# Performance work log

Measured on AMD Instinct MI355X. Metric: run time of the kernel, lower is better.

Reference implementation:

```python
import jax, jax.numpy as jnp
import numpy as np

MAX_POS = 512  # hardcoded max_pos_emb in the module
LN_EPS = 1e-5


def setup_inputs() -> dict:
    key = jax.random.key(0)
    ks = jax.random.split(key, 6)
    bs, n, d = 16, 4000, 1024
    h, dh = 8, 128
    inner = h * dh
    return {
        "x": jax.random.normal(ks[0], (bs, n, d), jnp.float32),
        "ln_w": jnp.ones((d,), jnp.float32),
        "ln_b": jnp.zeros((d,), jnp.float32),
        "Wq": (jax.random.normal(ks[1], (inner, d), jnp.float32) * 0.02),
        "Wkv": (jax.random.normal(ks[2], (2 * inner, d), jnp.float32) * 0.02),
        "Wo": (jax.random.normal(ks[3], (d, inner), jnp.float32) * 0.02),
        "bo": jnp.zeros((d,), jnp.float32),
        "rel_emb": (jax.random.normal(ks[4], (2 * MAX_POS + 1, dh), jnp.float32) * 0.02),
        "context_size": 256,
    }


def reference(x, ln_w, ln_b, Wq, Wkv, Wo, bo, rel_emb, context_size):
    bs, n, d = x.shape
    dh = rel_emb.shape[1]
    h = Wq.shape[0] // dh
    scale = dh ** -0.5
    cs = int(context_size)
    nb = -(-n // cs)          # ceil(n / cs)
    nr = n % cs

    # pre_norm (LayerNorm)
    mu = jnp.mean(x, axis=-1, keepdims=True)
    var = jnp.var(x, axis=-1, keepdims=True)
    xn = (x - mu) * jax.lax.rsqrt(var + LN_EPS) * ln_w + ln_b
    if nr > 0:
        xn = jnp.pad(xn, ((0, 0), (0, cs - nr), (0, 0)))

    q = xn @ Wq.T                    # (bs, nb*cs, h*dh)
    k, v = jnp.split(xn @ Wkv.T, 2, axis=-1)

    def blk(t):  # -> (bs, nb, h, cs, dh)
        return t.reshape(bs, nb, cs, h, dh).transpose(0, 1, 3, 2, 4)

    q, k, v = blk(q), blk(k), blk(v)

    # relative position bias, computed as a GEMM instead of broadcast-mul-sum
    seq = jnp.arange(cs)
    dist = jnp.clip(seq[:, None] - seq[None, :], -cs, cs) + MAX_POS
    rel = rel_emb[dist]                                     # (cs, cs, dh)
    pos_attn = jnp.einsum('bnhid,ijd->bnhij', q, rel) * scale

    if nr > 0:
        m = np.ones((cs, cs), dtype=bool)
        m[:nr, :nr] = False
        neg = -jnp.finfo(pos_attn.dtype).max
        pos_attn = pos_attn.at[:, -1].set(
            jnp.where(jnp.asarray(m), neg, pos_attn[:, -1]))

    # SDPA with additive mask: softmax(q k^T * scale + pos_attn) v
    scores = jnp.einsum('bnhid,bnhjd->bnhij', q, k) * scale + pos_attn
    attn = jax.nn.softmax(scores, axis=-1)
    out = jnp.einsum('bnhij,bnhjd->bnhid', attn, v)         # (bs, nb, h, cs, dh)

    out = out.transpose(0, 1, 3, 2, 4).reshape(bs, nb * cs, h * dh)[:, :n]
    return out @ Wo.T + bo  # dropout is identity in eval
```

## Files before the change

kernel.cpp:

```cpp
#include <hip/hip_runtime.h>

typedef __bf16 bf16;
typedef __bf16 bf16x8 __attribute__((ext_vector_type(8)));
typedef float f32x4 __attribute__((ext_vector_type(4)));

#define MFMA16(A,B,C) __builtin_amdgcn_mfma_f32_16x16x32_bf16(A,B,C,0,0,0)
#define SCALE 0.08838834764831843f
#define NEGBIG (-1e30f)

#define AS1(p) ((__attribute__((address_space(1))) void*)(p))
#define AS3(p) ((__attribute__((address_space(3))) void*)(p))

#define BAR() do { asm volatile("" ::: "memory"); __builtin_amdgcn_s_barrier(); asm volatile("" ::: "memory"); } while (0)

__global__ void cvt_bf16(const float* __restrict__ src, bf16* __restrict__ dst, int n) {
    int i = (blockIdx.x * 256 + threadIdx.x) * 4;
    if (i < n) {
        float4 v = *(const float4*)(src + i);
        dst[i + 0] = (bf16)v.x; dst[i + 1] = (bf16)v.y;
        dst[i + 2] = (bf16)v.z; dst[i + 3] = (bf16)v.w;
    }
}

__global__ __launch_bounds__(256) void ln_kernel(const float* __restrict__ x,
                                                 const float* __restrict__ w,
                                                 const float* __restrict__ b,
                                                 bf16* __restrict__ xn) {
    int row = blockIdx.x;
    int bb = row >> 12, p = row & 4095;
    int t = threadIdx.x;
    bf16* out = xn + ((size_t)row << 10);
    if (p >= 4000) {
        uint2 z; z.x = 0u; z.y = 0u;
        *(uint2*)(out + t * 4) = z;
        return;
    }
    float4 v = *(const float4*)(x + (((size_t)bb * 4000 + p) << 10) + t * 4);
    float s = v.x + v.y + v.z + v.w;
    float s2 = v.x * v.x + v.y * v.y + v.z * v.z + v.w * v.w;
#pragma unroll
    for (int m = 1; m < 64; m <<= 1) { s += __shfl_xor(s, m); s2 += __shfl_xor(s2, m); }
    __shared__ float red[8];
    int wv = t >> 6, l = t & 63;
    if (l == 0) { red[wv] = s; red[4 + wv] = s2; }
    __syncthreads();
    s = red[0] + red[1] + red[2] + red[3];
    s2 = red[4] + red[5] + red[6] + red[7];
    float mu = s * (1.f / 1024.f);
    float var = s2 * (1.f / 1024.f) - mu * mu;
    float inv = rsqrtf(var + 1e-5f);
    float4 wv4 = *(const float4*)(w + t * 4);
    float4 bv4 = *(const float4*)(b + t * 4);
    union { bf16 h[4]; uint2 u; } o;
    o.h[0] = (bf16)((v.x - mu) * inv * wv4.x + bv4.x);
    o.h[1] = (bf16)((v.y - mu) * inv * wv4.y + bv4.y);
    o.h[2] = (bf16)((v.z - mu) * inv * wv4.z + bv4.z);
    o.h[3] = (bf16)((v.w - mu) * inv * wv4.w + bv4.w);
    *(uint2*)(out + t * 4) = o.u;
}


__device__ __forceinline__ void stage_half(const bf16* __restrict__ src, int srow, int K,
                                           int kofs, bf16* ldsb, int w, int l) {
#pragma unroll
    for (int r = 0; r < 2; ++r) {
        int rh = (r * 8 + w) * 8 + (l >> 3);
        int chunk = (l & 7) ^ (rh & 7);
        __builtin_amdgcn_global_load_lds(AS1(src + (size_t)(srow + rh) * K + kofs + chunk * 8),
                                         AS3(ldsb + (r * 8 + w) * 512), 16, 0, 0);
    }
}

__device__ __forceinline__ bf16x8 fragLD(const bf16* base, int row, int ks, int lk) {
    int ch = ((ks * 4 + lk) ^ (row & 7)) * 8;
    return *(const bf16x8*)(base + row * 64 + ch);
}

#define RDA(AF, base, mofs) \
    _Pragma("unroll") for (int m = 0; m < 4; ++m) \
    _Pragma("unroll") for (int ks = 0; ks < 2; ++ks) \
        AF[m][ks] = fragLD(base, rA + (mofs + m) * 16 + lrow, ks, lk);

#define RDB2(nb, base) \
    _Pragma("unroll") for (int n = 0; n < 2; ++n) \
    _Pragma("unroll") for (int ks = 0; ks < 2; ++ks) \
        bfr[(nb) + n][ks] = fragLD(base, rB + ((nb) + n) * 16 + lrow, ks, lk);

#define MM(mb, AF, nb) do { \
    __builtin_amdgcn_s_setprio(1); \
    _Pragma("unroll") for (int m = 0; m < 4; ++m) \
    _Pragma("unroll") for (int n = 0; n < 2; ++n) \
    _Pragma("unroll") for (int ks = 0; ks < 2; ++ks) \
        acc[(mb) + m][(nb) + n] = MFMA16(AF[m][ks], bfr[(nb) + n][ks], acc[(mb) + m][(nb) + n]); \
    __builtin_amdgcn_s_setprio(0); } while (0)

template <int EPI>
__global__ __launch_bounds__(512, 2) void gemm256(const bf16* __restrict__ A,
                                                  const bf16* __restrict__ B,
                                                  bf16* __restrict__ C,
                                                  float* __restrict__ Cf,
                                                  const float* __restrict__ bias,
                                                  int M, int N, int K) {
    __shared__ __align__(16) bf16 LA[2 * 16384];
    __shared__ __align__(16) bf16 LB[2 * 16384];
    const int t = threadIdx.x;
    const int w = t >> 6, l = t & 63;
    const int lrow = l & 15, lk = l >> 4;
    const int wrM = w >> 2, wn = w & 3;
    const int rA = wrM * 128, rB = wn * 64;

    const int nwg = gridDim.x, cpx = nwg >> 3;
    const int swz = ((int)blockIdx.x & 7) * cpx + ((int)blockIdx.x >> 3);
    const int nbk = N >> 8;
    const int m0 = (swz / nbk) * 256;
    const int n0 = (swz % nbk) * 256;

    bf16* LA0 = LA;          bf16* LB0 = LB;
    bf16* LA1 = LA + 16384;  bf16* LB1 = LB + 16384;

    f32x4 acc[8][4] = {};
    bf16x8 afL[4][2], afH[4][2], bfr[4][2];

    const int NT = K >> 6, NI = K >> 7;

    stage_half(B, n0,       K, 0,  LB0,        w, l);
    stage_half(B, n0 + 128, K, 0,  LB0 + 8192, w, l);
    stage_half(A, m0,       K, 0,  LA0,        w, l);
    stage_half(A, m0 + 128, K, 0,  LA0 + 8192, w, l);
    stage_half(B, n0,       K, 64, LB1,        w, l);
    stage_half(B, n0 + 128, K, 64, LB1 + 8192, w, l);
    stage_half(A, m0,       K, 64, LA1,        w, l);
    asm volatile("s_waitcnt vmcnt(6)" ::: "memory");
    BAR();

    for (int i = 0; i < NI; ++i) {
        const int kS1 = (2 * i + 1) << 6;
        const int t2 = 2 * i + 2, t3 = 2 * i + 3;
        const int kS2 = ((t2 < NT) ? t2 : NT - 1) << 6;
        const int kS3 = ((t3 < NT) ? t3 : NT - 1) << 6;

        RDA(afL, LA0, 0);
        if (wn < 2) { RDB2(0, LB0); RDB2(2, LB0); } else { RDB2(0, LB0); }
        stage_half(A, m0 + 128, K, kS1, LA1 + 8192, w, l);
        BAR();
        MM(0, afL, 0);
        BAR();
        if (wn >= 2) { RDB2(2, LB0); }
        stage_half(B, n0, K, kS2, LB0, w, l);
        BAR();
        MM(0, afL, 2);
        BAR();
        RDA(afH, LA0, 4);
        stage_half(B, n0 + 128, K, kS2, LB0 + 8192, w, l);
        BAR();
        MM(4, afH, 0);
        BAR();
        stage_half(A, m0, K, kS2, LA0, w, l);
        BAR();
        MM(4, afH, 2);
        asm volatile("s_waitcnt vmcnt(6)" ::: "memory");
        BAR();
        RDA(afL, LA1, 0);
        if (wn < 2) { RDB2(0, LB1); RDB2(2, LB1); } else { RDB2(0, LB1); }
        stage_half(A, m0 + 128, K, kS2, LA0 + 8192, w, l);
        BAR();
        MM(0, afL, 0);
        BAR();
        if (wn >= 2) { RDB2(2, LB1); }
        stage_half(B, n0, K, kS3, LB1, w, l);
        BAR();
        MM(0, afL, 2);
        BAR();
        RDA(afH, LA1, 4);
        stage_half(B, n0 + 128, K, kS3, LB1 + 8192, w, l);
        BAR();
        MM(4, afH, 0);
        BAR();
        stage_half(A, m0, K, kS3, LA1, w, l);
        BAR();
        MM(4, afH, 2);
        asm volatile("s_waitcnt vmcnt(6)" ::: "memory");
        BAR();
    }

    asm volatile("s_waitcnt vmcnt(0)" ::: "memory");

    if (EPI == 0) {
#pragma unroll
        for (int m = 0; m < 8; ++m)
#pragma unroll
            for (int r = 0; r < 4; ++r) {
                size_t row = (size_t)(m0 + rA + m * 16 + lk * 4 + r);
                bf16* dst = C + row * N + n0 + rB;
#pragma unroll
                for (int n = 0; n < 4; ++n) dst[n * 16 + lrow] = (bf16)acc[m][n][r];
            }
    } else {
#pragma unroll
        for (int m = 0; m < 8; ++m)
#pragma unroll
            for (int r = 0; r < 4; ++r) {
                int row = m0 + rA + m * 16 + lk * 4 + r;
                int p = row & 4095, bb2 = row >> 12;
                if (p < 4000) {
                    float* dst = Cf + ((size_t)bb2 * 4000 + p) * 1024 + n0 + rB;
#pragma unroll
                    for (int n = 0; n < 4; ++n)
                        dst[n * 16 + lrow] = acc[m][n][r] + bias[n0 + rB + n * 16 + lrow];
                }
            }
    }
}

__global__ __launch_bounds__(256, 2) void bias_skew(const bf16* __restrict__ qkv,
                                                    const bf16* __restrict__ relw,
                                                    bf16* __restrict__ skew) {
    int bidx = blockIdx.x;
    int g = bidx & 7, bb = bidx >> 3;
    int h = bb & 7, blkn = (bb >> 3) & 15, b = bb >> 7;
    int mrow0 = b * 4096 + blkn * 256 + g * 32;
    const int t = threadIdx.x, w = t >> 6, l = t & 63, lrow = l & 15, lk = l >> 4;
    __shared__ __align__(16) bf16 Qs[32 * 136];
    __shared__ __align__(16) bf16 Ws[32 * 520];

#pragma unroll
    for (int q = 0; q < 2; ++q) {
        int idx = q * 256 + t;
        int row = idx >> 4, c8 = idx & 15;
        bf16x8 v = *(const bf16x8*)(qkv + (size_t)(mrow0 + row) * 3072 + h * 128 + c8 * 8);
        *(bf16x8*)&Qs[row * 136 + c8 * 8] = v;
    }
    __syncthreads();

    f32x4 acc[2][8] = {};
#pragma unroll
    for (int ks = 0; ks < 4; ++ks) {
        bf16x8 aq0 = *(const bf16x8*)&Qs[lrow * 136 + ks * 32 + lk * 8];
        bf16x8 aq1 = *(const bf16x8*)&Qs[(16 + lrow) * 136 + ks * 32 + lk * 8];
#pragma unroll
        for (int ct = 0; ct < 8; ++ct) {
            int c = w * 128 + ct * 16 + lrow;
            bf16x8 br = *(const bf16x8*)(relw + (size_t)c * 128 + ks * 32 + lk * 8);
            acc[0][ct] = MFMA16(aq0, br, acc[0][ct]);
            acc[1][ct] = MFMA16(aq1, br, acc[1][ct]);
        }
    }
#pragma unroll
    for (int mt = 0; mt < 2; ++mt)
#pragma unroll
        for (int ct = 0; ct < 8; ++ct)
#pragma unroll
            for (int r = 0; r < 4; ++r)
                Ws[(mt * 16 + lk * 4 + r) * 520 + w * 128 + ct * 16 + lrow] =
                    (bf16)(acc[mt][ct][r] * SCALE);
    __syncthreads();

    int jt = t >> 6, ll = t & 63;
    bool last = (blkn == 15);
    const bf16 negbig = (bf16)NEGBIG;
    union { bf16 hh[32]; uint4 q4[4]; } ob;
#pragma unroll
    for (int e = 0; e < 32; ++e) {
        int mt = e >> 4, nt = (e >> 2) & 3, r = e & 3;
        int iloc = mt * 16 + (ll >> 4) * 4 + r;
        int j = jt * 64 + nt * 16 + (ll & 15);
        int ig = g * 32 + iloc;
        int c = ig - j + 255;
        bool masked = last && (ig >= 160 || j >= 160);
        ob.hh[e] = masked ? negbig : Ws[iloc * 520 + c];
    }
    uint4* dst = (uint4*)(skew + ((((size_t)bb * 8 + g) * 4 + jt) * 64 + ll) * 32);
#pragma unroll
    for (int qq = 0; qq < 4; ++qq) dst[qq] = ob.q4[qq];
}

__global__ __launch_bounds__(512, 2) void attn_kernel(const bf16* __restrict__ qkv,
                                                      const bf16* __restrict__ skew,
                                                      bf16* __restrict__ ao) {
    int bb = blockIdx.x;
    int h = bb & 7, blkn = (bb >> 3) & 15, b = bb >> 7;
    const int t = threadIdx.x, w = t >> 6, l = t & 63, lrow = l & 15, lk = l >> 4;
    size_t qrow0 = (size_t)(b * 4096 + blkn * 256);
    __shared__ __align__(16) bf16 Ks[64 * 136];
    __shared__ __align__(16) bf16 Vt[128 * 72];
    __shared__ __align__(16) bf16 Ps[8][32 * 72];

    int i0 = w * 32;
    bf16x8 aq[2][4];
#pragma unroll
    for (int mt = 0; mt < 2; ++mt)
#pragma unroll
        for (int ks = 0; ks < 4; ++ks)
            aq[mt][ks] = *(const bf16x8*)(qkv + (qrow0 + i0 + mt * 16 + lrow) * 3072 +
                                          h * 128 + ks * 32 + lk * 8);

    f32x4 o[2][8] = {};
    float mrun[2][4], lrun[2][4];
#pragma unroll
    for (int mt = 0; mt < 2; ++mt)
#pragma unroll
        for (int r = 0; r < 4; ++r) { mrun[mt][r] = NEGBIG; lrun[mt][r] = 0.f; }

    for (int jt = 0; jt < 4; ++jt) {
        __syncthreads();
#pragma unroll
        for (int q = 0; q < 2; ++q) {
            int idx = q * 512 + t;
            int row = idx >> 4, c8 = idx & 15;
            bf16x8 v = *(const bf16x8*)(qkv + (qrow0 + jt * 64 + row) * 3072 + 1024 +
                                        h * 128 + c8 * 8);
            *(bf16x8*)&Ks[row * 136 + c8 * 8] = v;
        }
#pragma unroll
        for (int q = 0; q < 2; ++q) {
            int idx = q * 512 + t;
            int row = idx >> 4, c8 = idx & 15;
            bf16x8 v = *(const bf16x8*)(qkv + (qrow0 + jt * 64 + row) * 3072 + 2048 +
                                        h * 128 + c8 * 8);
#pragma unroll
            for (int e = 0; e < 8; ++e) Vt[(c8 * 8 + e) * 72 + row] = v[e];
        }
        __syncthreads();

        f32x4 s[2][4] = {};
#pragma unroll
        for (int nt = 0; nt < 4; ++nt)
#pragma unroll
            for (int ks = 0; ks < 4; ++ks) {
                bf16x8 bk = *(const bf16x8*)&Ks[(nt * 16 + lrow) * 136 + ks * 32 + lk * 8];
                s[0][nt] = MFMA16(aq[0][ks], bk, s[0][nt]);
                s[1][nt] = MFMA16(aq[1][ks], bk, s[1][nt]);
            }

        bf16x8 sk[4];
        const bf16x8* sp = (const bf16x8*)(skew +
                            ((((size_t)bb * 8 + w) * 4 + jt) * 64 + l) * 32);
        sk[0] = sp[0]; sk[1] = sp[1]; sk[2] = sp[2]; sk[3] = sp[3];
        float sv[2][4][4];
#pragma unroll
        for (int mt = 0; mt < 2; ++mt)
#pragma unroll
            for (int nt = 0; nt < 4; ++nt)
#pragma unroll
                for (int r = 0; r < 4; ++r)
                    sv[mt][nt][r] = s[mt][nt][r] * SCALE +
                                    (float)sk[mt * 2 + (nt >> 1)][(nt & 1) * 4 + r];

#pragma unroll
        for (int mt = 0; mt < 2; ++mt)
#pragma unroll
            for (int r = 0; r < 4; ++r) {
                float mx = fmaxf(fmaxf(sv[mt][0][r], sv[mt][1][r]),
                                 fmaxf(sv[mt][2][r], sv[mt][3][r]));
#pragma unroll
                for (int d = 1; d < 16; d <<= 1) mx = fmaxf(mx, __shfl_xor(mx, d));
                float mold = mrun[mt][r];
                float mn = fmaxf(mold, mx);
                float corr = __expf(mold - mn);
                mrun[mt][r] = mn;
                float rs = 0.f;
#pragma unroll
                for (int nt = 0; nt < 4; ++nt) {
                    float e = __expf(sv[mt][nt][r] - mn);
                    sv[mt][nt][r] = e; rs += e;
                }
#pragma unroll
                for (int d = 1; d < 16; d <<= 1) rs += __shfl_xor(rs, d);
                lrun[mt][r] = lrun[mt][r] * corr + rs;
#pragma unroll
                for (int dt = 0; dt < 8; ++dt) o[mt][dt][r] *= corr;
            }

#pragma unroll
        for (int mt = 0; mt < 2; ++mt)
#pragma unroll
            for (int nt = 0; nt < 4; ++nt)
#pragma unroll
                for (int r = 0; r < 4; ++r)
                    Ps[w][(mt * 16 + lk * 4 + r) * 72 + nt * 16 + lrow] = (bf16)sv[mt][nt][r];

#pragma unroll
        for (int pks = 0; pks < 2; ++pks) {
            bf16x8 ap0 = *(const bf16x8*)&Ps[w][lrow * 72 + pks * 32 + lk * 8];
            bf16x8 ap1 = *(const bf16x8*)&Ps[w][(16 + lrow) * 72 + pks * 32 + lk * 8];
#pragma unroll
            for (int dt = 0; dt < 8; ++dt) {
                bf16x8 bv = *(const bf16x8*)&Vt[(dt * 16 + lrow) * 72 + pks * 32 + lk * 8];
                o[0][dt] = MFMA16(ap0, bv, o[0][dt]);
                o[1][dt] = MFMA16(ap1, bv, o[1][dt]);
            }
        }
    }

#pragma unroll
    for (int mt = 0; mt < 2; ++mt)
#pragma unroll
        for (int r = 0; r < 4; ++r) {
            float inv = 1.0f / lrun[mt][r];
            size_t arow = qrow0 + i0 + mt * 16 + lk * 4 + r;
            bf16* dst = ao + arow * 1024 + h * 128;
#pragma unroll
            for (int dt = 0; dt < 8; ++dt)
                dst[dt * 16 + lrow] = (bf16)(o[mt][dt][r] * inv);
        }
}

extern "C" void kernel_launch(void* const* d_in, const int* in_sizes, int n_in,
                              void* d_out, int out_size, void* d_ws, size_t ws_size,
                              hipStream_t stream) {
    const float* x   = (const float*)d_in[0];
    const float* lnw = (const float*)d_in[1];
    const float* lnb = (const float*)d_in[2];
    const float* Wq  = (const float*)d_in[3];
    const float* Wkv = (const float*)d_in[4];
    const float* Wo  = (const float*)d_in[5];
    const float* bo  = (const float*)d_in[6];
    const float* rel = (const float*)d_in[7];

    const size_t OFF_XN   = 0;
    const size_t OFF_QKV  = OFF_XN + 134217728ULL;
    const size_t OFF_SKEW = OFF_QKV + 402653184ULL;
    const size_t OFF_WCAT = OFF_SKEW + 268435456ULL;
    const size_t OFF_WO   = OFF_WCAT + 6291456ULL;
    const size_t OFF_RELW = OFF_WO + 2097152ULL;
    const size_t NEED     = OFF_RELW + 131072ULL;
    if (ws_size < NEED) return;

    char* ws = (char*)d_ws;
    bf16* xn   = (bf16*)(ws + OFF_XN);
    bf16* qkv  = (bf16*)(ws + OFF_QKV);
    bf16* skw  = (bf16*)(ws + OFF_SKEW);
    bf16* wcat = (bf16*)(ws + OFF_WCAT);
    bf16* wo   = (bf16*)(ws + OFF_WO);
    bf16* relw = (bf16*)(ws + OFF_RELW);
    bf16* ao   = xn;
    float* out = (float*)d_out;

    cvt_bf16<<<1024, 256, 0, stream>>>(Wq, wcat, 1048576);
    cvt_bf16<<<2048, 256, 0, stream>>>(Wkv, wcat + 1048576, 2097152);
    cvt_bf16<<<1024, 256, 0, stream>>>(Wo, wo, 1048576);
    cvt_bf16<<<64, 256, 0, stream>>>(rel + 257 * 128, relw, 65536);
    ln_kernel<<<65536, 256, 0, stream>>>(x, lnw, lnb, xn);
    gemm256<0><<<3072, 512, 0, stream>>>(xn, wcat, qkv, nullptr, nullptr, 65536, 3072, 1024);
    bias_skew<<<16384, 256, 0, stream>>>(qkv, relw, skw);
    attn_kernel<<<2048, 512, 0, stream>>>(qkv, skw, ao);
    gemm256<1><<<1024, 512, 0, stream>>>(ao, wo, nullptr, out, bo, 65536, 1024, 1024);
}
```

Measured before the change: 1.228 ms.

## Fuse relative-position bias GEMM into attention and prefetch K/V tiles

Removes the separate bias_skew kernel and its 256MB skew buffer. The attention kernel now computes the q·rel products per key tile with extra MFMAs into per-warp LDS, applies the skew and the padding mask inline, and reuses that LDS buffer for P. K/V loads for the next tile are prefetched into registers and held there while the current tile is computed. This cuts a large global write/read round trip at the cost of extra MFMA work and more register and LDS pressure in the attention kernel.

```diff
diff --git a/kernel.cpp b/kernel.cpp
--- a/kernel.cpp
+++ b/kernel.cpp
@@ -212,70 +212,8 @@
     }
 }
 
-__global__ __launch_bounds__(256, 2) void bias_skew(const bf16* __restrict__ qkv,
-                                                    const bf16* __restrict__ relw,
-                                                    bf16* __restrict__ skew) {
-    int bidx = blockIdx.x;
-    int g = bidx & 7, bb = bidx >> 3;
-    int h = bb & 7, blkn = (bb >> 3) & 15, b = bb >> 7;
-    int mrow0 = b * 4096 + blkn * 256 + g * 32;
-    const int t = threadIdx.x, w = t >> 6, l = t & 63, lrow = l & 15, lk = l >> 4;
-    __shared__ __align__(16) bf16 Qs[32 * 136];
-    __shared__ __align__(16) bf16 Ws[32 * 520];
-
-#pragma unroll
-    for (int q = 0; q < 2; ++q) {
-        int idx = q * 256 + t;
-        int row = idx >> 4, c8 = idx & 15;
-        bf16x8 v = *(const bf16x8*)(qkv + (size_t)(mrow0 + row) * 3072 + h * 128 + c8 * 8);
-        *(bf16x8*)&Qs[row * 136 + c8 * 8] = v;
-    }
-    __syncthreads();
-
-    f32x4 acc[2][8] = {};
-#pragma unroll
-    for (int ks = 0; ks < 4; ++ks) {
-        bf16x8 aq0 = *(const bf16x8*)&Qs[lrow * 136 + ks * 32 + lk * 8];
-        bf16x8 aq1 = *(const bf16x8*)&Qs[(16 + lrow) * 136 + ks * 32 + lk * 8];
-#pragma unroll
-        for (int ct = 0; ct < 8; ++ct) {
-            int c = w * 128 + ct * 16 + lrow;
-            bf16x8 br = *(const bf16x8*)(relw + (size_t)c * 128 + ks * 32 + lk * 8);
-            acc[0][ct] = MFMA16(aq0, br, acc[0][ct]);
-            acc[1][ct] = MFMA16(aq1, br, acc[1][ct]);
-        }
-    }
-#pragma unroll
-    for (int mt = 0; mt < 2; ++mt)
-#pragma unroll
-        for (int ct = 0; ct < 8; ++ct)
-#pragma unroll
-            for (int r = 0; r < 4; ++r)
-                Ws[(mt * 16 + lk * 4 + r) * 520 + w * 128 + ct * 16 + lrow] =
-                    (bf16)(acc[mt][ct][r] * SCALE);
-    __syncthreads();
-
-    int jt = t >> 6, ll = t & 63;
-    bool last = (blkn == 15);
-    const bf16 negbig = (bf16)NEGBIG;
-    union { bf16 hh[32]; uint4 q4[4]; } ob;
-#pragma unroll
-    for (int e = 0; e < 32; ++e) {
-        int mt = e >> 4, nt = (e >> 2) & 3, r = e & 3;
-        int iloc = mt * 16 + (ll >> 4) * 4 + r;
-        int j = jt * 64 + nt * 16 + (ll & 15);
-        int ig = g * 32 + iloc;
-        int c = ig - j + 255;
-        bool masked = last && (ig >= 160 || j >= 160);
-        ob.hh[e] = masked ? negbig : Ws[iloc * 520 + c];
-    }
-    uint4* dst = (uint4*)(skew + ((((size_t)bb * 8 + g) * 4 + jt) * 64 + ll) * 32);
-#pragma unroll
-    for (int qq = 0; qq < 4; ++qq) dst[qq] = ob.q4[qq];
-}
-
 __global__ __launch_bounds__(512, 2) void attn_kernel(const bf16* __restrict__ qkv,
-                                                      const bf16* __restrict__ skew,
+                                                      const bf16* __restrict__ relw,
                                                       bf16* __restrict__ ao) {
     int bb = blockIdx.x;
     int h = bb & 7, blkn = (bb >> 3) & 15, b = bb >> 7;
@@ -283,9 +221,12 @@
     size_t qrow0 = (size_t)(b * 4096 + blkn * 256);
     __shared__ __align__(16) bf16 Ks[64 * 136];
     __shared__ __align__(16) bf16 Vt[128 * 72];
-    __shared__ __align__(16) bf16 Ps[8][32 * 72];
-
-    int i0 = w * 32;
+    __shared__ __align__(16) bf16 Wps[8][32 * 96];
+
+    const int i0 = w * 32;
+    const bool last = (blkn == 15);
+    const int srow = t >> 4, sc8 = t & 15;
+
     bf16x8 aq[2][4];
 #pragma unroll
     for (int mt = 0; mt < 2; ++mt)
@@ -301,26 +242,32 @@
 #pragma unroll
         for (int r = 0; r < 4; ++r) { mrun[mt][r] = NEGBIG; lrun[mt][r] = 0.f; }
 
+    bf16x8 kreg[2], vreg[2];
+#pragma unroll
+    for (int q = 0; q < 2; ++q) {
+        int row = q * 32 + srow;
+        kreg[q] = *(const bf16x8*)(qkv + (qrow0 + row) * 3072 + 1024 + h * 128 + sc8 * 8);
+        vreg[q] = *(const bf16x8*)(qkv + (qrow0 + row) * 3072 + 2048 + h * 128 + sc8 * 8);
+    }
+#pragma unroll
+    for (int q = 0; q < 2; ++q) {
+        int row = q * 32 + srow;
+        *(bf16x8*)&Ks[row * 136 + sc8 * 8] = kreg[q];
+#pragma unroll
+        for (int e = 0; e < 8; ++e) Vt[(sc8 * 8 + e) * 72 + row] = vreg[q][e];
+    }
+    __syncthreads();
+
     for (int jt = 0; jt < 4; ++jt) {
-        __syncthreads();
-#pragma unroll
-        for (int q = 0; q < 2; ++q) {
-            int idx = q * 512 + t;
-            int row = idx >> 4, c8 = idx & 15;
-            bf16x8 v = *(const bf16x8*)(qkv + (qrow0 + jt * 64 + row) * 3072 + 1024 +
-                                        h * 128 + c8 * 8);
-            *(bf16x8*)&Ks[row * 136 + c8 * 8] = v;
+        if (jt < 3) {
+#pragma unroll
+            for (int q = 0; q < 2; ++q) {
+                int row = (jt + 1) * 64 + q * 32 + srow;
+                kreg[q] = *(const bf16x8*)(qkv + (qrow0 + row) * 3072 + 1024 + h * 128 + sc8 * 8);
+                vreg[q] = *(const bf16x8*)(qkv + (qrow0 + row) * 3072 + 2048 + h * 128 + sc8 * 8);
+            }
+            asm volatile("" ::: "memory");
         }
-#pragma unroll
-        for (int q = 0; q < 2; ++q) {
-            int idx = q * 512 + t;
-            int row = idx >> 4, c8 = idx & 15;
-            bf16x8 v = *(const bf16x8*)(qkv + (qrow0 + jt * 64 + row) * 3072 + 2048 +
-                                        h * 128 + c8 * 8);
-#pragma unroll
-            for (int e = 0; e < 8; ++e) Vt[(c8 * 8 + e) * 72 + row] = v[e];
-        }
-        __syncthreads();
 
         f32x4 s[2][4] = {};
 #pragma unroll
@@ -332,19 +279,40 @@
                 s[1][nt] = MFMA16(aq[1][ks], bk, s[1][nt]);
             }
 
-        bf16x8 sk[4];
-        const bf16x8* sp = (const bf16x8*)(skew +
-                            ((((size_t)bb * 8 + w) * 4 + jt) * 64 + l) * 32);
-        sk[0] = sp[0]; sk[1] = sp[1]; sk[2] = sp[2]; sk[3] = sp[3];
+        const int cbase = i0 - jt * 64 + 192;
+        f32x4 wacc[2][6] = {};
+#pragma unroll
+        for (int ks = 0; ks < 4; ++ks)
+#pragma unroll
+            for (int ct = 0; ct < 6; ++ct) {
+                bf16x8 br = *(const bf16x8*)(relw + (size_t)(cbase + ct * 16 + lrow) * 128 +
+                                             ks * 32 + lk * 8);
+                wacc[0][ct] = MFMA16(aq[0][ks], br, wacc[0][ct]);
+                wacc[1][ct] = MFMA16(aq[1][ks], br, wacc[1][ct]);
+            }
+        bf16* wb = &Wps[w][0];
+#pragma unroll
+        for (int mt = 0; mt < 2; ++mt)
+#pragma unroll
+            for (int ct = 0; ct < 6; ++ct)
+#pragma unroll
+                for (int r = 0; r < 4; ++r)
+                    wb[(mt * 16 + lk * 4 + r) * 96 + ct * 16 + lrow] = (bf16)wacc[mt][ct][r];
+
         float sv[2][4][4];
 #pragma unroll
         for (int mt = 0; mt < 2; ++mt)
 #pragma unroll
             for (int nt = 0; nt < 4; ++nt)
 #pragma unroll
-                for (int r = 0; r < 4; ++r)
-                    sv[mt][nt][r] = s[mt][nt][r] * SCALE +
-                                    (float)sk[mt * 2 + (nt >> 1)][(nt & 1) * 4 + r];
+                for (int r = 0; r < 4; ++r) {
+                    int row = mt * 16 + lk * 4 + r;
+                    int cc = row - nt * 16 - lrow + 63;
+                    float xv = (s[mt][nt][r] + (float)wb[row * 96 + cc]) * SCALE;
+                    if (last && (i0 + row >= 160 || jt * 64 + nt * 16 + lrow >= 160))
+                        xv = NEGBIG;
+                    sv[mt][nt][r] = xv;
+                }
 
 #pragma unroll
         for (int mt = 0; mt < 2; ++mt)
@@ -371,18 +339,19 @@
                 for (int dt = 0; dt < 8; ++dt) o[mt][dt][r] *= corr;
             }
 
+        bf16* ps = &Wps[w][0];
 #pragma unroll
         for (int mt = 0; mt < 2; ++mt)
 #pragma unroll
             for (int nt = 0; nt < 4; ++nt)
 #pragma unroll
                 for (int r = 0; r < 4; ++r)
-                    Ps[w][(mt * 16 + lk * 4 + r) * 72 + nt * 16 + lrow] = (bf16)sv[mt][nt][r];
+                    ps[(mt * 16 + lk * 4 + r) * 72 + nt * 16 + lrow] = (bf16)sv[mt][nt][r];
 
 #pragma unroll
         for (int pks = 0; pks < 2; ++pks) {
-            bf16x8 ap0 = *(const bf16x8*)&Ps[w][lrow * 72 + pks * 32 + lk * 8];
-            bf16x8 ap1 = *(const bf16x8*)&Ps[w][(16 + lrow) * 72 + pks * 32 + lk * 8];
+            bf16x8 ap0 = *(const bf16x8*)&ps[lrow * 72 + pks * 32 + lk * 8];
+            bf16x8 ap1 = *(const bf16x8*)&ps[(16 + lrow) * 72 + pks * 32 + lk * 8];
 #pragma unroll
             for (int dt = 0; dt < 8; ++dt) {
                 bf16x8 bv = *(const bf16x8*)&Vt[(dt * 16 + lrow) * 72 + pks * 32 + lk * 8];
@@ -390,6 +359,18 @@
                 o[1][dt] = MFMA16(ap1, bv, o[1][dt]);
             }
         }
+
+        __syncthreads();
+        if (jt < 3) {
+#pragma unroll
+            for (int q = 0; q < 2; ++q) {
+                int row = q * 32 + srow;
+                *(bf16x8*)&Ks[row * 136 + sc8 * 8] = kreg[q];
+#pragma unroll
+                for (int e = 0; e < 8; ++e) Vt[(sc8 * 8 + e) * 72 + row] = vreg[q][e];
+            }
+        }
+        __syncthreads();
     }
 
 #pragma unroll
@@ -419,8 +400,7 @@
 
     const size_t OFF_XN   = 0;
     const size_t OFF_QKV  = OFF_XN + 134217728ULL;
-    const size_t OFF_SKEW = OFF_QKV + 402653184ULL;
-    const size_t OFF_WCAT = OFF_SKEW + 268435456ULL;
+    const size_t OFF_WCAT = OFF_QKV + 402653184ULL;
     const size_t OFF_WO   = OFF_WCAT + 6291456ULL;
     const size_t OFF_RELW = OFF_WO + 2097152ULL;
     const size_t NEED     = OFF_RELW + 131072ULL;
@@ -429,7 +409,6 @@
     char* ws = (char*)d_ws;
     bf16* xn   = (bf16*)(ws + OFF_XN);
     bf16* qkv  = (bf16*)(ws + OFF_QKV);
-    bf16* skw  = (bf16*)(ws + OFF_SKEW);
     bf16* wcat = (bf16*)(ws + OFF_WCAT);
     bf16* wo   = (bf16*)(ws + OFF_WO);
     bf16* relw = (bf16*)(ws + OFF_RELW);
@@ -442,7 +421,6 @@
     cvt_bf16<<<64, 256, 0, stream>>>(rel + 257 * 128, relw, 65536);
     ln_kernel<<<65536, 256, 0, stream>>>(x, lnw, lnb, xn);
     gemm256<0><<<3072, 512, 0, stream>>>(xn, wcat, qkv, nullptr, nullptr, 65536, 3072, 1024);
-    bias_skew<<<16384, 256, 0, stream>>>(qkv, relw, skw);
-    attn_kernel<<<2048, 512, 0, stream>>>(qkv, skw, ao);
+    attn_kernel<<<2048, 512, 0, stream>>>(qkv, relw, ao);
     gemm256<1><<<1024, 512, 0, stream>>>(ao, wo, nullptr, out, bo, 65536, 1024, 1024);
 }
```

Result: no change. 1.234 ms (+0.5%).
